# Performance work log

Hardware: AMD Instinct MI355X
Metric: run time of the kernel (lower is better)

Reference implementation:

```python
import jax, jax.numpy as jnp
import numpy as np

B, N, DIM, H, DH = 2, 2048, 512, 8, 64
INNER = H * DH


def setup_inputs() -> dict:
    key = jax.random.key(0)
    ks = jax.random.split(key, 6)
    x = jax.random.normal(ks[0], (B, N, DIM), dtype=jnp.float32)
    mask_np = jax.random.randint(ks[1], (B, N), 0, 2, dtype=jnp.int32)
    mask_bert = jax.random.randint(ks[2], (B, N), 0, 2, dtype=jnp.int32)
    # params (torch Linear(dim, 3*inner, bias=False) -> stored here as [in, out])
    s_in = 1.0 / np.sqrt(DIM)
    s_inner = 1.0 / np.sqrt(INNER)
    W_qkv = jax.random.uniform(ks[3], (DIM, 3 * INNER), jnp.float32, -s_in, s_in)
    W_out = jax.random.uniform(ks[4], (INNER, DIM), jnp.float32, -s_inner, s_inner)
    b_out = jax.random.uniform(ks[5], (DIM,), jnp.float32, -s_inner, s_inner)
    return {"x": x, "mask_np": mask_np, "mask_bert": mask_bert,
            "W_qkv": W_qkv, "W_out": W_out, "b_out": b_out}


def reference(x, mask_np, mask_bert, W_qkv, W_out, b_out):
    scale = DH ** -0.5
    qkv = x @ W_qkv                                   # [b, n, 3*inner]
    q, k, v = jnp.split(qkv, 3, axis=-1)
    split_heads = lambda t: t.reshape(B, N, H, DH).transpose(0, 2, 1, 3)  # b h n d
    q, k, v = split_heads(q), split_heads(k), split_heads(v)
    dots = jnp.einsum('bhid,bhjd->bhij', q, k) * scale  # [b, h, n, n]
    # dual mask: (np_i * np_j == 0) or (bert_j == 1) -> fill with -1000
    np_pair = mask_np[:, None, :, None] * mask_np[:, None, None, :]      # b 1 n n
    bert_j = mask_bert[:, None, None, :]                                  # b 1 1 n
    masked = (np_pair == 0) | (bert_j == 1)
    dots = jnp.where(masked, jnp.float32(-1000.0), dots)
    attn = jax.nn.softmax(dots, axis=-1)
    out = jnp.einsum('bhij,bhjd->bhid', attn, v)       # b h n d
    out = out.transpose(0, 2, 1, 3).reshape(B, N, INNER)
    return out @ W_out + b_out
```

## Files before the change

### kernel.cpp

```cpp
#include <hip/hip_runtime.h>

typedef __attribute__((ext_vector_type(8))) short short8;
typedef __attribute__((ext_vector_type(4))) float f32x4;

#define GLDS16(gp, lp)                                                                     \
  __builtin_amdgcn_global_load_lds(                                                        \
      (const __attribute__((address_space(1))) unsigned int*)(gp),                         \
      (__attribute__((address_space(3))) unsigned int*)(lp), 16, 0, 0)

__device__ __forceinline__ unsigned short f2bf(float f) {
  unsigned u = __float_as_uint(f);
  u += 0x7FFFu + ((u >> 16) & 1u);
  return (unsigned short)(u >> 16);
}
__device__ __forceinline__ float bf2f(unsigned short h) {
  return __uint_as_float(((unsigned)h) << 16);
}
__device__ __forceinline__ unsigned cvt_pk_bf16(float a, float b) {
  unsigned r;
  asm("v_cvt_pk_bf16_f32 %0, %1, %2" : "=v"(r) : "v"(a), "v"(b));
  return r;
}

__global__ __launch_bounds__(256) void prep_x(
    const float* __restrict__ x, const int* __restrict__ mnp, const int* __restrict__ mbert,
    unsigned short* __restrict__ xb, float* __restrict__ jmflt) {
  int tid = blockIdx.x * 256 + threadIdx.x;
  if (tid < 524288) {
    float4 v = *(const float4*)(x + tid * 4);
    ushort4 o;
    o.x = f2bf(v.x); o.y = f2bf(v.y); o.z = f2bf(v.z); o.w = f2bf(v.w);
    *(ushort4*)(xb + tid * 4) = o;
  } else {
    int o = tid - 524288;
    if (o < 4096) jmflt[o] = (mnp[o] == 0 || mbert[o] == 1) ? -64.0f : 1e30f;
  }
}

__global__ __launch_bounds__(256) void transpose_w(
    const float* __restrict__ wqkv, const float* __restrict__ wout,
    unsigned short* __restrict__ wqkvT, unsigned short* __restrict__ whiT,
    unsigned short* __restrict__ wloT) {
  __shared__ float tile[64][65];
  int bid = blockIdx.x;
  const float* src;
  int N, k0, n0, which;
  if (bid < 192) { which = 0; src = wqkv; N = 1536; k0 = (bid / 24) * 64; n0 = (bid % 24) * 64; }
  else { bid -= 192; which = 1; src = wout; N = 512; k0 = (bid / 8) * 64; n0 = (bid % 8) * 64; }
  int tx = threadIdx.x & 63, ty = threadIdx.x >> 6;
#pragma unroll
  for (int i = 0; i < 16; ++i) {
    int row = ty + i * 4;
    tile[row][tx] = src[(k0 + row) * N + n0 + tx];
  }
  __syncthreads();
#pragma unroll
  for (int i = 0; i < 16; ++i) {
    int row = ty + i * 4;
    float w = tile[tx][row];
    if (which == 0) {
      wqkvT[(n0 + row) * 512 + k0 + tx] = f2bf(w);
    } else {
      unsigned short hi = f2bf(w);
      whiT[(n0 + row) * 512 + k0 + tx] = hi;
      wloT[(n0 + row) * 512 + k0 + tx] = f2bf(w - bf2f(hi));
    }
  }
}

__global__ __launch_bounds__(256) void qkv_gemm(
    const unsigned short* __restrict__ A, const unsigned short* __restrict__ Bt,
    unsigned short* __restrict__ qb, unsigned short* __restrict__ kb,
    unsigned short* __restrict__ vtb) {
  __shared__ __attribute__((aligned(16))) unsigned short lA[64 * 64];
  __shared__ __attribute__((aligned(16))) unsigned short lB[128 * 64];
  const int lane = threadIdx.x & 63, wid = threadIdx.x >> 6;
  const int l15 = lane & 15, lg = lane >> 4;
  const int row0 = blockIdx.x * 64;
  const int col0 = blockIdx.y * 128;
  const int srow = lane >> 3;
  const int gslot = (lane & 7) ^ srow;
  f32x4 acc[4][2] = {};

  for (int ks = 0; ks < 8; ++ks) {
    const int k0 = ks * 64;
    __syncthreads();
#pragma unroll
    for (int i = 0; i < 2; ++i) {
      int c = wid * 2 + i;
      GLDS16(A + (row0 + c * 8 + srow) * 512 + k0 + gslot * 8, lA + c * 512);
    }
#pragma unroll
    for (int i = 0; i < 4; ++i) {
      int c = wid * 4 + i;
      GLDS16(Bt + (col0 + c * 8 + srow) * 512 + k0 + gslot * 8, lB + c * 512);
    }
    __syncthreads();
#pragma unroll
    for (int ksub = 0; ksub < 2; ++ksub) {
      short8 af[4], bfr[2];
#pragma unroll
      for (int m = 0; m < 4; ++m) {
        int row = m * 16 + l15;
        int slot = (ksub * 4 + lg) ^ (row & 7);
        af[m] = *(const short8*)(lA + row * 64 + slot * 8);
      }
#pragma unroll
      for (int n = 0; n < 2; ++n) {
        int row = wid * 32 + n * 16 + l15;
        int slot = (ksub * 4 + lg) ^ (row & 7);
        bfr[n] = *(const short8*)(lB + row * 64 + slot * 8);
      }
#pragma unroll
      for (int m = 0; m < 4; ++m)
#pragma unroll
        for (int n = 0; n < 2; ++n)
          acc[m][n] = __builtin_amdgcn_mfma_f32_16x16x32_bf16(af[m], bfr[n], acc[m][n], 0, 0, 0);
    }
  }
#pragma unroll
  for (int m = 0; m < 4; ++m) {
#pragma unroll
    for (int n = 0; n < 2; ++n) {
      int col = col0 + wid * 32 + n * 16 + l15;
      int which = col >> 9, hh = (col >> 6) & 7, d = col & 63;
#pragma unroll
      for (int r = 0; r < 4; ++r) {
        int grow = row0 + m * 16 + lg * 4 + r;
        int b = grow >> 11, np = grow & 2047;
        float v = acc[m][n][r];
        if (which == 0)
          qb[((b * 8 + hh) * 2048 + np) * 64 + d] = f2bf(v * 0.125f);
        else if (which == 1)
          kb[((b * 8 + hh) * 2048 + np) * 64 + d] = f2bf(v);
        else
          vtb[((b * 8 + hh) * 64 + d) * 2048 + np] = f2bf(v);
      }
    }
  }
}

__global__ __launch_bounds__(256) void attn_kernel(
    const unsigned short* __restrict__ qg, const unsigned short* __restrict__ kg,
    const unsigned short* __restrict__ vtg, const int* __restrict__ mnp,
    const float* __restrict__ jmflt,
    unsigned short* __restrict__ ahi, unsigned short* __restrict__ alo) {
  __shared__ __attribute__((aligned(16))) unsigned short Kbuf[2][64 * 64];
  __shared__ __attribute__((aligned(16))) unsigned short Vbuf[2][64 * 64];
  __shared__ __attribute__((aligned(16))) float jmlds[2048];
  __shared__ __attribute__((aligned(16))) unsigned short Plds[4][16 * 72];
  const int lane = threadIdx.x & 63, wid = threadIdx.x >> 6;
  const int l15 = lane & 15, lg = lane >> 4;
  const int srow = lane >> 3, gslot = (lane & 7) ^ srow;
  const int bh = blockIdx.x, b = bh >> 3, h = bh & 7;
  const int q0 = blockIdx.y * 64 + wid * 16;
  const unsigned short* Q = qg + bh * (2048 * 64);
  const unsigned short* K = kg + bh * (2048 * 64);
  const unsigned short* VT = vtg + bh * (64 * 2048);

#pragma unroll
  for (int i = 0; i < 2; ++i)
    GLDS16(jmflt + b * 2048 + wid * 512 + i * 256 + lane * 4, jmlds + wid * 512 + i * 256);
#pragma unroll
  for (int i = 0; i < 2; ++i)
    GLDS16(K + (wid * 16 + i * 8 + srow) * 64 + gslot * 8, &Kbuf[0][(wid * 16 + i * 8) * 64]);
#pragma unroll
  for (int i = 0; i < 2; ++i)
    GLDS16(VT + (wid * 16 + i * 8 + srow) * 2048 + gslot * 8, &Vbuf[0][(wid * 16 + i * 8) * 64]);

  short8 qf[2];
#pragma unroll
  for (int s = 0; s < 2; ++s)
    qf[s] = *(const short8*)(Q + (q0 + l15) * 64 + s * 32 + lg * 8);
  const float rowflt = (mnp[b * 2048 + q0 + l15] == 0) ? -64.0f : 1e30f;

  f32x4 accO[4] = {};
  float psum = 0.0f;
  unsigned short* Pl = &Plds[wid][0];
  int cur = 0;

  for (int jt = 0; jt < 32; ++jt) {
    const int j0 = jt * 64;
    if (jt < 31) {
      const int jn = j0 + 64;
      const int nb = cur ^ 1;
#pragma unroll
      for (int i = 0; i < 2; ++i)
        GLDS16(K + (jn + wid * 16 + i * 8 + srow) * 64 + gslot * 8,
               &Kbuf[nb][(wid * 16 + i * 8) * 64]);
#pragma unroll
      for (int i = 0; i < 2; ++i)
        GLDS16(VT + (wid * 16 + i * 8 + srow) * 2048 + jn + gslot * 8,
               &Vbuf[nb][(wid * 16 + i * 8) * 64]);
      asm volatile("s_waitcnt vmcnt(4)" ::: "memory");
    } else {
      asm volatile("s_waitcnt vmcnt(0)" ::: "memory");
    }
    __builtin_amdgcn_s_barrier();

    short8 kf[4][2], vf[4][2];
    f32x4 jm[4];
    const int sw = (l15 & 7) * 8;
#pragma unroll
    for (int t = 0; t < 4; ++t) {
      const int row = t * 16 + l15;
#pragma unroll
      for (int s = 0; s < 2; ++s)
        kf[t][s] = *(const short8*)(&Kbuf[cur][row * 64 + ((s * 32 + lg * 8) ^ sw)]);
      jm[t] = *(const f32x4*)(&jmlds[j0 + t * 16 + lg * 4]);
    }
#pragma unroll
    for (int dt = 0; dt < 4; ++dt) {
      const int row = dt * 16 + l15;
#pragma unroll
      for (int c = 0; c < 2; ++c)
        vf[dt][c] = *(const short8*)(&Vbuf[cur][row * 64 + ((c * 32 + lg * 8) ^ sw)]);
    }

    f32x4 sacc[4] = {};
#pragma unroll
    for (int t = 0; t < 4; ++t)
#pragma unroll
      for (int s = 0; s < 2; ++s)
        sacc[t] = __builtin_amdgcn_mfma_f32_16x16x32_bf16(kf[t][s], qf[s], sacc[t], 0, 0, 0);

#pragma unroll
    for (int t = 0; t < 4; ++t) {
      float e[4];
#pragma unroll
      for (int r = 0; r < 4; ++r) {
        float sv = fminf(fminf(sacc[t][r], jm[t][r]), rowflt);
        e[r] = __expf(sv);
        psum += e[r];
      }
      unsigned p01 = cvt_pk_bf16(e[0], e[1]);
      unsigned p23 = cvt_pk_bf16(e[2], e[3]);
      *(unsigned*)(Pl + l15 * 72 + t * 16 + lg * 4 + 0) = p01;
      *(unsigned*)(Pl + l15 * 72 + t * 16 + lg * 4 + 2) = p23;
    }
    short8 pa[2];
#pragma unroll
    for (int c = 0; c < 2; ++c)
      pa[c] = *(const short8*)(Pl + l15 * 72 + c * 32 + lg * 8);
#pragma unroll
    for (int dt = 0; dt < 4; ++dt)
#pragma unroll
      for (int c = 0; c < 2; ++c)
        accO[dt] = __builtin_amdgcn_mfma_f32_16x16x32_bf16(pa[c], vf[dt][c], accO[dt], 0, 0, 0);

    __builtin_amdgcn_s_barrier();
    cur ^= 1;
  }

  psum += __shfl_xor(psum, 16);
  psum += __shfl_xor(psum, 32);
  float lsum[4];
#pragma unroll
  for (int r = 0; r < 4; ++r) lsum[r] = __shfl(psum, lg * 4 + r);
#pragma unroll
  for (int dt = 0; dt < 4; ++dt) {
#pragma unroll
    for (int r = 0; r < 4; ++r) {
      float val = accO[dt][r] / lsum[r];
      int row = q0 + lg * 4 + r;
      int col = h * 64 + dt * 16 + l15;
      unsigned short hi = f2bf(val);
      ahi[(b * 2048 + row) * 512 + col] = hi;
      alo[(b * 2048 + row) * 512 + col] = f2bf(val - bf2f(hi));
    }
  }
}

__global__ __launch_bounds__(256) void outproj_gemm(
    const unsigned short* __restrict__ Ahi, const unsigned short* __restrict__ Alo,
    const unsigned short* __restrict__ WhiT, const unsigned short* __restrict__ WloT,
    const float* __restrict__ bias, float* __restrict__ out) {
  __shared__ __attribute__((aligned(16))) unsigned short lA[32 * 64];
  __shared__ __attribute__((aligned(16))) unsigned short lB[128 * 64];
  const int lane = threadIdx.x & 63, wid = threadIdx.x >> 6;
  const int l15 = lane & 15, lg = lane >> 4;
  const int row0 = blockIdx.x * 32;
  const int col0 = blockIdx.y * 128;
  const int srow = lane >> 3;
  const int gslot = (lane & 7) ^ srow;
  f32x4 acc[2][2] = {};

  for (int ks = 0; ks < 24; ++ks) {
    const int seg = ks >> 3;
    const int k0 = (ks & 7) * 64;
    const unsigned short* Asrc = (seg == 1) ? Alo : Ahi;
    const unsigned short* Bsrc = (seg == 2) ? WloT : WhiT;
    __syncthreads();
    GLDS16(Asrc + (row0 + wid * 8 + srow) * 512 + k0 + gslot * 8, lA + wid * 512);
#pragma unroll
    for (int i = 0; i < 4; ++i) {
      int c = wid * 4 + i;
      GLDS16(Bsrc + (col0 + c * 8 + srow) * 512 + k0 + gslot * 8, lB + c * 512);
    }
    __syncthreads();
#pragma unroll
    for (int ksub = 0; ksub < 2; ++ksub) {
      short8 af[2], bfr[2];
#pragma unroll
      for (int m = 0; m < 2; ++m) {
        int row = m * 16 + l15;
        int slot = (ksub * 4 + lg) ^ (row & 7);
        af[m] = *(const short8*)(lA + row * 64 + slot * 8);
      }
#pragma unroll
      for (int n = 0; n < 2; ++n) {
        int row = wid * 32 + n * 16 + l15;
        int slot = (ksub * 4 + lg) ^ (row & 7);
        bfr[n] = *(const short8*)(lB + row * 64 + slot * 8);
      }
#pragma unroll
      for (int m = 0; m < 2; ++m)
#pragma unroll
        for (int n = 0; n < 2; ++n)
          acc[m][n] = __builtin_amdgcn_mfma_f32_16x16x32_bf16(af[m], bfr[n], acc[m][n], 0, 0, 0);
    }
  }
#pragma unroll
  for (int m = 0; m < 2; ++m) {
#pragma unroll
    for (int n = 0; n < 2; ++n) {
      int col = col0 + wid * 32 + n * 16 + l15;
      float bb = bias[col];
#pragma unroll
      for (int r = 0; r < 4; ++r) {
        int grow = row0 + m * 16 + lg * 4 + r;
        out[grow * 512 + col] = acc[m][n][r] + bb;
      }
    }
  }
}

extern "C" void kernel_launch(void* const* d_in, const int* in_sizes, int n_in,
                              void* d_out, int out_size, void* d_ws, size_t ws_size,
                              hipStream_t stream) {
  (void)in_sizes; (void)n_in; (void)out_size; (void)ws_size;
  const float* x = (const float*)d_in[0];
  const int* mnp = (const int*)d_in[1];
  const int* mbert = (const int*)d_in[2];
  const float* wqkv = (const float*)d_in[3];
  const float* wout = (const float*)d_in[4];
  const float* bout = (const float*)d_in[5];
  float* out = (float*)d_out;

  char* ws = (char*)d_ws;
  size_t off = 0;
  auto alloc = [&](size_t bytes) {
    void* p = ws + off;
    off += (bytes + 255) & ~(size_t)255;
    return p;
  };
  unsigned short* xb    = (unsigned short*)alloc(2097152 * 2);
  unsigned short* wqkvT = (unsigned short*)alloc(786432 * 2);
  unsigned short* qb    = (unsigned short*)alloc(2097152 * 2);
  unsigned short* kb    = (unsigned short*)alloc(2097152 * 2);
  unsigned short* vtb   = (unsigned short*)alloc(2097152 * 2);
  unsigned short* ahi   = (unsigned short*)alloc(2097152 * 2);
  unsigned short* alo   = (unsigned short*)alloc(2097152 * 2);
  unsigned short* whiT  = (unsigned short*)alloc(262144 * 2);
  unsigned short* wloT  = (unsigned short*)alloc(262144 * 2);
  float* jmflt          = (float*)alloc(4096 * 4);

  prep_x<<<2064, 256, 0, stream>>>(x, mnp, mbert, xb, jmflt);
  transpose_w<<<256, 256, 0, stream>>>(wqkv, wout, wqkvT, whiT, wloT);
  qkv_gemm<<<dim3(64, 12), 256, 0, stream>>>(xb, wqkvT, qb, kb, vtb);
  attn_kernel<<<dim3(16, 32), 256, 0, stream>>>(qb, kb, vtb, mnp, jmflt, ahi, alo);
  outproj_gemm<<<dim3(128, 4), 256, 0, stream>>>(ahi, alo, whiT, wloT, bout, out);
}
```

Before: 141.7 us.

## Double-buffer GEMM loads, deepen attention prefetch, coalesce V^T stores, use exp2

```diff
diff --git a/kernel.cpp b/kernel.cpp
--- a/kernel.cpp
+++ b/kernel.cpp
@@ -22,9 +22,11 @@
   return r;
 }
 
+#define QSCALE 0.1803368801111244f
+
 __global__ __launch_bounds__(256) void prep_x(
     const float* __restrict__ x, const int* __restrict__ mnp, const int* __restrict__ mbert,
-    unsigned short* __restrict__ xb, float* __restrict__ jmflt) {
+    unsigned short* __restrict__ xb, unsigned short* __restrict__ jmbf) {
   int tid = blockIdx.x * 256 + threadIdx.x;
   if (tid < 524288) {
     float4 v = *(const float4*)(x + tid * 4);
@@ -33,7 +35,7 @@
     *(ushort4*)(xb + tid * 4) = o;
   } else {
     int o = tid - 524288;
-    if (o < 4096) jmflt[o] = (mnp[o] == 0 || mbert[o] == 1) ? -64.0f : 1e30f;
+    if (o < 4096) jmbf[o] = (mnp[o] == 0 || mbert[o] == 1) ? f2bf(-100.0f) : f2bf(1e30f);
   }
 }
 
@@ -72,8 +74,8 @@
     const unsigned short* __restrict__ A, const unsigned short* __restrict__ Bt,
     unsigned short* __restrict__ qb, unsigned short* __restrict__ kb,
     unsigned short* __restrict__ vtb) {
-  __shared__ __attribute__((aligned(16))) unsigned short lA[64 * 64];
-  __shared__ __attribute__((aligned(16))) unsigned short lB[128 * 64];
+  __shared__ __attribute__((aligned(16))) unsigned short lA[2][64 * 64];
+  __shared__ __attribute__((aligned(16))) unsigned short lB[2][128 * 64];
   const int lane = threadIdx.x & 63, wid = threadIdx.x >> 6;
   const int l15 = lane & 15, lg = lane >> 4;
   const int row0 = blockIdx.x * 64;
@@ -82,20 +84,31 @@
   const int gslot = (lane & 7) ^ srow;
   f32x4 acc[4][2] = {};
 
+#define QKV_STAGE(ks_, buf_)                                                               \
+  {                                                                                        \
+    const int k0_ = (ks_) * 64;                                                            \
+    _Pragma("unroll") for (int i = 0; i < 2; ++i) {                                        \
+      int c = wid * 2 + i;                                                                 \
+      GLDS16(A + (row0 + c * 8 + srow) * 512 + k0_ + gslot * 8, &lA[buf_][c * 512]);       \
+    }                                                                                      \
+    _Pragma("unroll") for (int i = 0; i < 4; ++i) {                                        \
+      int c = wid * 4 + i;                                                                 \
+      GLDS16(Bt + (col0 + c * 8 + srow) * 512 + k0_ + gslot * 8, &lB[buf_][c * 512]);      \
+    }                                                                                      \
+  }
+
+  QKV_STAGE(0, 0);
+  int buf = 0;
   for (int ks = 0; ks < 8; ++ks) {
-    const int k0 = ks * 64;
-    __syncthreads();
-#pragma unroll
-    for (int i = 0; i < 2; ++i) {
-      int c = wid * 2 + i;
-      GLDS16(A + (row0 + c * 8 + srow) * 512 + k0 + gslot * 8, lA + c * 512);
-    }
-#pragma unroll
-    for (int i = 0; i < 4; ++i) {
-      int c = wid * 4 + i;
-      GLDS16(Bt + (col0 + c * 8 + srow) * 512 + k0 + gslot * 8, lB + c * 512);
-    }
-    __syncthreads();
+    if (ks < 7) {
+      QKV_STAGE(ks + 1, buf ^ 1);
+      asm volatile("s_waitcnt vmcnt(6)" ::: "memory");
+    } else {
+      asm volatile("s_waitcnt vmcnt(0)" ::: "memory");
+    }
+    __builtin_amdgcn_s_barrier();
+    const unsigned short* La = &lA[buf][0];
+    const unsigned short* Lb = &lB[buf][0];
 #pragma unroll
     for (int ksub = 0; ksub < 2; ++ksub) {
       short8 af[4], bfr[2];
@@ -103,13 +116,13 @@
       for (int m = 0; m < 4; ++m) {
         int row = m * 16 + l15;
         int slot = (ksub * 4 + lg) ^ (row & 7);
-        af[m] = *(const short8*)(lA + row * 64 + slot * 8);
+        af[m] = *(const short8*)(La + row * 64 + slot * 8);
       }
 #pragma unroll
       for (int n = 0; n < 2; ++n) {
         int row = wid * 32 + n * 16 + l15;
         int slot = (ksub * 4 + lg) ^ (row & 7);
-        bfr[n] = *(const short8*)(lB + row * 64 + slot * 8);
+        bfr[n] = *(const short8*)(Lb + row * 64 + slot * 8);
       }
 #pragma unroll
       for (int m = 0; m < 4; ++m)
@@ -117,24 +130,48 @@
         for (int n = 0; n < 2; ++n)
           acc[m][n] = __builtin_amdgcn_mfma_f32_16x16x32_bf16(af[m], bfr[n], acc[m][n], 0, 0, 0);
     }
-  }
-#pragma unroll
-  for (int m = 0; m < 4; ++m) {
-#pragma unroll
-    for (int n = 0; n < 2; ++n) {
-      int col = col0 + wid * 32 + n * 16 + l15;
-      int which = col >> 9, hh = (col >> 6) & 7, d = col & 63;
-#pragma unroll
-      for (int r = 0; r < 4; ++r) {
-        int grow = row0 + m * 16 + lg * 4 + r;
-        int b = grow >> 11, np = grow & 2047;
-        float v = acc[m][n][r];
-        if (which == 0)
-          qb[((b * 8 + hh) * 2048 + np) * 64 + d] = f2bf(v * 0.125f);
-        else if (which == 1)
-          kb[((b * 8 + hh) * 2048 + np) * 64 + d] = f2bf(v);
-        else
-          vtb[((b * 8 + hh) * 64 + d) * 2048 + np] = f2bf(v);
+    __builtin_amdgcn_s_barrier();
+    buf ^= 1;
+  }
+
+  if (col0 >= 1024) {
+    unsigned short* T = &lB[0][0];
+#pragma unroll
+    for (int m = 0; m < 4; ++m)
+#pragma unroll
+      for (int n = 0; n < 2; ++n) {
+        int lc = wid * 32 + n * 16 + l15;
+#pragma unroll
+        for (int r = 0; r < 4; ++r)
+          T[lc * 72 + m * 16 + lg * 4 + r] = f2bf(acc[m][n][r]);
+      }
+    __syncthreads();
+    int c = threadIdx.x >> 1, half = threadIdx.x & 1;
+    int gcol = col0 + c;
+    int hh = (gcol >> 6) & 7, d = gcol & 63;
+    int b = row0 >> 11, np0 = row0 & 2047;
+    unsigned short* dst = vtb + ((size_t)((b * 8 + hh) * 64 + d)) * 2048 + np0 + half * 32;
+    const unsigned short* srcT = T + c * 72 + half * 32;
+#pragma unroll
+    for (int i = 0; i < 4; ++i)
+      *(short8*)(dst + i * 8) = *(const short8*)(srcT + i * 8);
+  } else {
+#pragma unroll
+    for (int m = 0; m < 4; ++m) {
+#pragma unroll
+      for (int n = 0; n < 2; ++n) {
+        int col = col0 + wid * 32 + n * 16 + l15;
+        int which = col >> 9, hh = (col >> 6) & 7, d = col & 63;
+#pragma unroll
+        for (int r = 0; r < 4; ++r) {
+          int grow = row0 + m * 16 + lg * 4 + r;
+          int b = grow >> 11, np = grow & 2047;
+          float v = acc[m][n][r];
+          if (which == 0)
+            qb[((b * 8 + hh) * 2048 + np) * 64 + d] = f2bf(v * QSCALE);
+          else
+            kb[((b * 8 + hh) * 2048 + np) * 64 + d] = f2bf(v);
+        }
       }
     }
   }
@@ -143,11 +180,11 @@
 __global__ __launch_bounds__(256) void attn_kernel(
     const unsigned short* __restrict__ qg, const unsigned short* __restrict__ kg,
     const unsigned short* __restrict__ vtg, const int* __restrict__ mnp,
-    const float* __restrict__ jmflt,
+    const unsigned short* __restrict__ jmbf,
     unsigned short* __restrict__ ahi, unsigned short* __restrict__ alo) {
-  __shared__ __attribute__((aligned(16))) unsigned short Kbuf[2][64 * 64];
-  __shared__ __attribute__((aligned(16))) unsigned short Vbuf[2][64 * 64];
-  __shared__ __attribute__((aligned(16))) float jmlds[2048];
+  __shared__ __attribute__((aligned(16))) unsigned short Kbuf[4][64 * 64];
+  __shared__ __attribute__((aligned(16))) unsigned short Vbuf[4][64 * 64];
+  __shared__ __attribute__((aligned(16))) unsigned short jmlds[2048];
   __shared__ __attribute__((aligned(16))) unsigned short Plds[4][16 * 72];
   const int lane = threadIdx.x & 63, wid = threadIdx.x >> 6;
   const int l15 = lane & 15, lg = lane >> 4;
@@ -158,63 +195,60 @@
   const unsigned short* K = kg + bh * (2048 * 64);
   const unsigned short* VT = vtg + bh * (64 * 2048);
 
-#pragma unroll
-  for (int i = 0; i < 2; ++i)
-    GLDS16(jmflt + b * 2048 + wid * 512 + i * 256 + lane * 4, jmlds + wid * 512 + i * 256);
-#pragma unroll
-  for (int i = 0; i < 2; ++i)
-    GLDS16(K + (wid * 16 + i * 8 + srow) * 64 + gslot * 8, &Kbuf[0][(wid * 16 + i * 8) * 64]);
-#pragma unroll
-  for (int i = 0; i < 2; ++i)
-    GLDS16(VT + (wid * 16 + i * 8 + srow) * 2048 + gslot * 8, &Vbuf[0][(wid * 16 + i * 8) * 64]);
+#define ATTN_STAGE(jt_, buf_)                                                              \
+  {                                                                                        \
+    const int jb_ = (jt_) * 64;                                                            \
+    _Pragma("unroll") for (int i = 0; i < 2; ++i)                                          \
+        GLDS16(K + (jb_ + wid * 16 + i * 8 + srow) * 64 + gslot * 8,                       \
+               &Kbuf[buf_][(wid * 16 + i * 8) * 64]);                                      \
+    _Pragma("unroll") for (int i = 0; i < 2; ++i)                                          \
+        GLDS16(VT + (wid * 16 + i * 8 + srow) * 2048 + jb_ + gslot * 8,                    \
+               &Vbuf[buf_][(wid * 16 + i * 8) * 64]);                                      \
+  }
+
+  GLDS16(jmbf + b * 2048 + wid * 512 + lane * 8, jmlds + wid * 512);
+  ATTN_STAGE(0, 0);
+  ATTN_STAGE(1, 1);
 
   short8 qf[2];
 #pragma unroll
   for (int s = 0; s < 2; ++s)
     qf[s] = *(const short8*)(Q + (q0 + l15) * 64 + s * 32 + lg * 8);
-  const float rowflt = (mnp[b * 2048 + q0 + l15] == 0) ? -64.0f : 1e30f;
+  const float rowflt = (mnp[b * 2048 + q0 + l15] == 0) ? -100.0f : 1e30f;
 
   f32x4 accO[4] = {};
   float psum = 0.0f;
   unsigned short* Pl = &Plds[wid][0];
-  int cur = 0;
 
   for (int jt = 0; jt < 32; ++jt) {
-    const int j0 = jt * 64;
-    if (jt < 31) {
-      const int jn = j0 + 64;
-      const int nb = cur ^ 1;
-#pragma unroll
-      for (int i = 0; i < 2; ++i)
-        GLDS16(K + (jn + wid * 16 + i * 8 + srow) * 64 + gslot * 8,
-               &Kbuf[nb][(wid * 16 + i * 8) * 64]);
-#pragma unroll
-      for (int i = 0; i < 2; ++i)
-        GLDS16(VT + (wid * 16 + i * 8 + srow) * 2048 + jn + gslot * 8,
-               &Vbuf[nb][(wid * 16 + i * 8) * 64]);
+    if (jt < 30) {
+      ATTN_STAGE(jt + 2, (jt + 2) & 3);
+      asm volatile("s_waitcnt vmcnt(8)" ::: "memory");
+    } else if (jt == 30) {
       asm volatile("s_waitcnt vmcnt(4)" ::: "memory");
     } else {
       asm volatile("s_waitcnt vmcnt(0)" ::: "memory");
     }
     __builtin_amdgcn_s_barrier();
 
+    const unsigned short* Kc = &Kbuf[jt & 3][0];
+    const unsigned short* Vc = &Vbuf[jt & 3][0];
+    const int j0 = jt * 64;
+    const int sw = (l15 & 7) * 8;
     short8 kf[4][2], vf[4][2];
-    f32x4 jm[4];
-    const int sw = (l15 & 7) * 8;
 #pragma unroll
     for (int t = 0; t < 4; ++t) {
       const int row = t * 16 + l15;
 #pragma unroll
       for (int s = 0; s < 2; ++s)
-        kf[t][s] = *(const short8*)(&Kbuf[cur][row * 64 + ((s * 32 + lg * 8) ^ sw)]);
-      jm[t] = *(const f32x4*)(&jmlds[j0 + t * 16 + lg * 4]);
+        kf[t][s] = *(const short8*)(&Kc[row * 64 + ((s * 32 + lg * 8) ^ sw)]);
     }
 #pragma unroll
     for (int dt = 0; dt < 4; ++dt) {
       const int row = dt * 16 + l15;
 #pragma unroll
       for (int c = 0; c < 2; ++c)
-        vf[dt][c] = *(const short8*)(&Vbuf[cur][row * 64 + ((c * 32 + lg * 8) ^ sw)]);
+        vf[dt][c] = *(const short8*)(&Vc[row * 64 + ((c * 32 + lg * 8) ^ sw)]);
     }
 
     f32x4 sacc[4] = {};
@@ -226,17 +260,17 @@
 
 #pragma unroll
     for (int t = 0; t < 4; ++t) {
+      ushort4 jmv = *(const ushort4*)(&jmlds[j0 + t * 16 + lg * 4]);
+      float jmf[4] = {bf2f(jmv.x), bf2f(jmv.y), bf2f(jmv.z), bf2f(jmv.w)};
       float e[4];
 #pragma unroll
       for (int r = 0; r < 4; ++r) {
-        float sv = fminf(fminf(sacc[t][r], jm[t][r]), rowflt);
-        e[r] = __expf(sv);
+        float sv = fminf(fminf(sacc[t][r], jmf[r]), rowflt);
+        e[r] = exp2f(sv);
         psum += e[r];
       }
-      unsigned p01 = cvt_pk_bf16(e[0], e[1]);
-      unsigned p23 = cvt_pk_bf16(e[2], e[3]);
-      *(unsigned*)(Pl + l15 * 72 + t * 16 + lg * 4 + 0) = p01;
-      *(unsigned*)(Pl + l15 * 72 + t * 16 + lg * 4 + 2) = p23;
+      *(unsigned*)(Pl + l15 * 72 + t * 16 + lg * 4 + 0) = cvt_pk_bf16(e[0], e[1]);
+      *(unsigned*)(Pl + l15 * 72 + t * 16 + lg * 4 + 2) = cvt_pk_bf16(e[2], e[3]);
     }
     short8 pa[2];
 #pragma unroll
@@ -247,21 +281,18 @@
 #pragma unroll
       for (int c = 0; c < 2; ++c)
         accO[dt] = __builtin_amdgcn_mfma_f32_16x16x32_bf16(pa[c], vf[dt][c], accO[dt], 0, 0, 0);
-
-    __builtin_amdgcn_s_barrier();
-    cur ^= 1;
   }
 
   psum += __shfl_xor(psum, 16);
   psum += __shfl_xor(psum, 32);
   float lsum[4];
 #pragma unroll
-  for (int r = 0; r < 4; ++r) lsum[r] = __shfl(psum, lg * 4 + r);
+  for (int r = 0; r < 4; ++r) lsum[r] = 1.0f / __shfl(psum, lg * 4 + r);
 #pragma unroll
   for (int dt = 0; dt < 4; ++dt) {
 #pragma unroll
     for (int r = 0; r < 4; ++r) {
-      float val = accO[dt][r] / lsum[r];
+      float val = accO[dt][r] * lsum[r];
       int row = q0 + lg * 4 + r;
       int col = h * 64 + dt * 16 + l15;
       unsigned short hi = f2bf(val);
@@ -275,8 +306,8 @@
     const unsigned short* __restrict__ Ahi, const unsigned short* __restrict__ Alo,
     const unsigned short* __restrict__ WhiT, const unsigned short* __restrict__ WloT,
     const float* __restrict__ bias, float* __restrict__ out) {
-  __shared__ __attribute__((aligned(16))) unsigned short lA[32 * 64];
-  __shared__ __attribute__((aligned(16))) unsigned short lB[128 * 64];
+  __shared__ __attribute__((aligned(16))) unsigned short lA[2][32 * 64];
+  __shared__ __attribute__((aligned(16))) unsigned short lB[2][128 * 64];
   const int lane = threadIdx.x & 63, wid = threadIdx.x >> 6;
   const int l15 = lane & 15, lg = lane >> 4;
   const int row0 = blockIdx.x * 32;
@@ -285,19 +316,31 @@
   const int gslot = (lane & 7) ^ srow;
   f32x4 acc[2][2] = {};
 
+#define OP_STAGE(ks_, buf_)                                                                \
+  {                                                                                        \
+    const int seg_ = (ks_) >> 3;                                                           \
+    const int k0_ = ((ks_) & 7) * 64;                                                      \
+    const unsigned short* Asrc_ = (seg_ == 1) ? Alo : Ahi;                                 \
+    const unsigned short* Bsrc_ = (seg_ == 2) ? WloT : WhiT;                               \
+    GLDS16(Asrc_ + (row0 + wid * 8 + srow) * 512 + k0_ + gslot * 8, &lA[buf_][wid * 512]); \
+    _Pragma("unroll") for (int i = 0; i < 4; ++i) {                                        \
+      int c = wid * 4 + i;                                                                 \
+      GLDS16(Bsrc_ + (col0 + c * 8 + srow) * 512 + k0_ + gslot * 8, &lB[buf_][c * 512]);   \
+    }                                                                                      \
+  }
+
+  OP_STAGE(0, 0);
+  int buf = 0;
   for (int ks = 0; ks < 24; ++ks) {
-    const int seg = ks >> 3;
-    const int k0 = (ks & 7) * 64;
-    const unsigned short* Asrc = (seg == 1) ? Alo : Ahi;
-    const unsigned short* Bsrc = (seg == 2) ? WloT : WhiT;
-    __syncthreads();
-    GLDS16(Asrc + (row0 + wid * 8 + srow) * 512 + k0 + gslot * 8, lA + wid * 512);
-#pragma unroll
-    for (int i = 0; i < 4; ++i) {
-      int c = wid * 4 + i;
-      GLDS16(Bsrc + (col0 + c * 8 + srow) * 512 + k0 + gslot * 8, lB + c * 512);
-    }
-    __syncthreads();
+    if (ks < 23) {
+      OP_STAGE(ks + 1, buf ^ 1);
+      asm volatile("s_waitcnt vmcnt(5)" ::: "memory");
+    } else {
+      asm volatile("s_waitcnt vmcnt(0)" ::: "memory");
+    }
+    __builtin_amdgcn_s_barrier();
+    const unsigned short* La = &lA[buf][0];
+    const unsigned short* Lb = &lB[buf][0];
 #pragma unroll
     for (int ksub = 0; ksub < 2; ++ksub) {
       short8 af[2], bfr[2];
@@ -305,13 +348,13 @@
       for (int m = 0; m < 2; ++m) {
         int row = m * 16 + l15;
         int slot = (ksub * 4 + lg) ^ (row & 7);
-        af[m] = *(const short8*)(lA + row * 64 + slot * 8);
+        af[m] = *(const short8*)(La + row * 64 + slot * 8);
       }
 #pragma unroll
       for (int n = 0; n < 2; ++n) {
         int row = wid * 32 + n * 16 + l15;
         int slot = (ksub * 4 + lg) ^ (row & 7);
-        bfr[n] = *(const short8*)(lB + row * 64 + slot * 8);
+        bfr[n] = *(const short8*)(Lb + row * 64 + slot * 8);
       }
 #pragma unroll
       for (int m = 0; m < 2; ++m)
@@ -319,6 +362,8 @@
         for (int n = 0; n < 2; ++n)
           acc[m][n] = __builtin_amdgcn_mfma_f32_16x16x32_bf16(af[m], bfr[n], acc[m][n], 0, 0, 0);
     }
+    __builtin_amdgcn_s_barrier();
+    buf ^= 1;
   }
 #pragma unroll
   for (int m = 0; m < 2; ++m) {
@@ -363,11 +408,11 @@
   unsigned short* alo   = (unsigned short*)alloc(2097152 * 2);
   unsigned short* whiT  = (unsigned short*)alloc(262144 * 2);
   unsigned short* wloT  = (unsigned short*)alloc(262144 * 2);
-  float* jmflt          = (float*)alloc(4096 * 4);
-
-  prep_x<<<2064, 256, 0, stream>>>(x, mnp, mbert, xb, jmflt);
+  unsigned short* jmbf  = (unsigned short*)alloc(4096 * 2);
+
+  prep_x<<<2064, 256, 0, stream>>>(x, mnp, mbert, xb, jmbf);
   transpose_w<<<256, 256, 0, stream>>>(wqkv, wout, wqkvT, whiT, wloT);
   qkv_gemm<<<dim3(64, 12), 256, 0, stream>>>(xb, wqkvT, qb, kb, vtb);
-  attn_kernel<<<dim3(16, 32), 256, 0, stream>>>(qb, kb, vtb, mnp, jmflt, ahi, alo);
+  attn_kernel<<<dim3(16, 32), 256, 0, stream>>>(qb, kb, vtb, mnp, jmbf, ahi, alo);
   outproj_gemm<<<dim3(128, 4), 256, 0, stream>>>(ahi, alo, whiT, wloT, bout, out);
 }
```

Result: no change. 144.1 us (+1.7%).
